# Kernel tuning notes

Measured on AMD Instinct MI355X. Metric: run time of the kernel, lower is better.

Reference implementation:

```python
import jax, jax.numpy as jnp
import numpy as np

B, IC, OC, K, H, W = 16, 16, 64, 3, 256, 256


def setup_inputs() -> dict:
    key = jax.random.key(0)
    k1, k2, k3 = jax.random.split(key, 3)
    x = jax.random.normal(k1, (B, IC, H, W), dtype=jnp.float32)
    # nn.Conv2d default init: uniform(-1/sqrt(fan_in), 1/sqrt(fan_in))
    bound = 1.0 / np.sqrt(IC * K * K)
    weight = jax.random.uniform(k2, (OC, IC, K, K), jnp.float32, -bound, bound)
    bias = jax.random.uniform(k3, (OC,), jnp.float32, -bound, bound)
    return {"x": x, "weight": weight, "bias": bias}


def reference(x, weight, bias):
    """Fused 'conv-window multiply -> min over (oc, kh, kw, ic) -> +bias -> tanh(tanh(.))'.

    Matches the CUDA kernel: for each output pixel it takes
        min over (oc, kh, kw, ic) of  x_pad[b, ic, h+kh, w+kw] * w[oc, ic, kh, kw] + bias[oc]
    (bias[oc] is constant within an oc, so folding it into the joint min is exact),
    then applies tanh twice. Output is [B, 1, H, W]; out-of-bounds taps use x=0
    (stride=1, padding=0 per the conv state, but the kernel still writes HxW).
    """
    b_, ic_, h_, w_ = x.shape
    oc_, _, k_, _ = weight.shape
    # zero-pad on the high side only: ih = ph + kh can reach H + K - 2
    xp = jnp.pad(x, ((0, 0), (0, 0), (0, k_ - 1), (0, k_ - 1)))

    # ---- pass 1: find the argmin index over the joint (oc, kh, kw, ic) axis ----
    xs = jax.lax.stop_gradient(xp)
    ws = jax.lax.stop_gradient(weight)
    bs = jax.lax.stop_gradient(bias)
    big = jnp.asarray(np.finfo(np.float32).max, jnp.float32)  # FLT_MAX as in kernel

    def body(carry, inp):
        best, bestj = carry                      # [B,H,W] f32, [B,H,W] i32
        wk, bk, oc = inp                         # [IC,K,K], scalar, i32
        for kh in range(k_):
            for kw in range(k_):
                win = xs[:, :, kh:kh + h_, kw:kw + w_]          # [B,IC,H,W]
                v = win * wk[None, :, kh, kw, None, None] + bk   # [B,IC,H,W]
                vm = jnp.min(v, axis=1)                          # [B,H,W]
                ici = jnp.argmin(v, axis=1).astype(jnp.int32)    # [B,H,W]
                jj = ((oc * k_ + kh) * k_ + kw) * ic_ + ici
                better = vm < best
                best = jnp.where(better, vm, best)
                bestj = jnp.where(better, jj, bestj)
        return (best, bestj), None

    init = (jnp.full((b_, h_, w_), big, jnp.float32),
            jnp.zeros((b_, h_, w_), jnp.int32))
    (_, bestj), _ = jax.lax.scan(body, init, (ws, bs, jnp.arange(oc_, dtype=jnp.int32)))

    # ---- pass 2: differentiable gather of the winning tap ----
    ic = bestj % ic_
    t = bestj // ic_
    kw = t % k_
    t = t // k_
    kh = t % k_
    oc = t // k_
    bi = jnp.arange(b_)[:, None, None]
    hi = jnp.arange(h_)[None, :, None]
    wi = jnp.arange(w_)[None, None, :]
    xv = xp[bi, ic, hi + kh, wi + kw]            # [B,H,W]
    wv = weight[oc, ic, kh, kw]                  # [B,H,W]
    out = jnp.tanh(jnp.tanh(xv * wv + bias[oc]))
    return out[:, None, :, :]                    # [B,1,H,W]
```

## Files before the change

kernel.cpp:

```cpp
#include <hip/hip_runtime.h>
#include <cmath>

constexpr int Bn = 16, ICn = 16, OCn = 64, Kn = 3, Hn = 256, Wn = 256;
constexpr int NE   = ICn * Kn * Kn;
constexpr int CAPF = 16;
constexpr int CNT_OFF   = 0;
constexpr int FLAG_OFF  = 256;
constexpr int LINES_OFF = 4096;

constexpr double XLIM = 16.0;

typedef float v2f __attribute__((ext_vector_type(2)));

__global__ void build_hulls(const float* __restrict__ weight,
                            const float* __restrict__ bias,
                            unsigned int* __restrict__ counts,
                            int* __restrict__ flag,
                            float2* __restrict__ lines)
{
    int wave = (int)(threadIdx.x >> 6);
    int lane = (int)(threadIdx.x & 63);
    int e = blockIdx.x * 4 + wave;
    if (e >= NE) return;
    int ic = e / (Kn * Kn);
    int t  = e % (Kn * Kn);

    double mm = (double)weight[((size_t)lane * ICn + ic) * (Kn * Kn) + t];
    double cc = (double)bias[lane];

    double v_cur = mm * (-XLIM) + cc;
    double m_cur = mm, c_cur = cc;
    #pragma unroll
    for (int off = 32; off >= 1; off >>= 1) {
        double v2 = __shfl_xor(v_cur, off, 64);
        double m2 = __shfl_xor(m_cur, off, 64);
        double c2 = __shfl_xor(c_cur, off, 64);
        if (v2 < v_cur || (v2 == v_cur && m2 < m_cur)) {
            v_cur = v2; m_cur = m2; c_cur = c2;
        }
    }

    float2* L = lines + (size_t)e * CAPF;
    int n = 0;
    while (true) {
        if (lane == 0 && n < CAPF) L[n] = make_float2((float)m_cur, (float)c_cur);
        ++n;
        double xi = 1e308, mi = 0.0, ci = 0.0;
        if (mm < m_cur) {
            xi = (cc - c_cur) / (m_cur - mm);
            mi = mm; ci = cc;
        }
        #pragma unroll
        for (int off = 32; off >= 1; off >>= 1) {
            double x2 = __shfl_xor(xi, off, 64);
            double m2 = __shfl_xor(mi, off, 64);
            double c2 = __shfl_xor(ci, off, 64);
            if (x2 < xi || (x2 == xi && (m2 < mi || (m2 == mi && c2 < ci)))) {
                xi = x2; mi = m2; ci = c2;
            }
        }
        if (xi >= XLIM) break;
        m_cur = mi; c_cur = ci;
    }
    if (lane == 0) {
        if (n > CAPF) { atomicOr(flag, 1); n = CAPF; }
        int np = (n + 3) & ~3;
        float2 last = L[n - 1];
        for (int p = n; p < np; ++p) L[p] = last;
        unsigned int g = (unsigned int)(np >> 2);
        atomicOr(&counts[ic * 2 + (t >> 3)], g << ((t & 7) * 4));
    }
}

__device__ __forceinline__ v2f vmin3(v2f a, v2f b, v2f c) {
    v2f r;
    r.x = fminf(a.x, fminf(b.x, c.x));
    r.y = fminf(a.y, fminf(b.y, c.y));
    return r;
}

__global__ __launch_bounds__(256) void fused_min_tanh4(
    const float* __restrict__ x,
    const unsigned int* __restrict__ counts,
    const int* __restrict__ flag,
    const float4* __restrict__ linesg,
    const float* __restrict__ weight,
    const float* __restrict__ bias,
    float* __restrict__ out)
{
    __shared__ float4 S[NE * (CAPF / 2)];
    __shared__ unsigned int Scw[32];

    const int tid = (int)threadIdx.x;
    for (int k = tid; k < NE * (CAPF / 2); k += 256) S[k] = linesg[k];
    if (tid < 32) Scw[tid] = counts[tid];
    __syncthreads();

    const int row  = (int)blockIdx.x * 4 + (tid >> 6);
    const int b0   = row >> 8;
    const int h    = row & 255;
    const int lane = tid & 63;
    const int w0   = lane << 2;
    const bool tail = (lane == 63);

    v2f A0, A1, A2, A3;
    A0.x = 3.4e38f; A0.y = 3.4e38f; A1 = A0; A2 = A0; A3 = A0;

    const float* xb = x + (size_t)b0 * (ICn * Hn * Wn);

    if (*flag == 0) {
        #pragma unroll 1
        for (int ic = 0; ic < ICn; ++ic) {
            const float* xc = xb + ic * (Hn * Wn);
            float r[3][6];
            #pragma unroll
            for (int kh = 0; kh < 3; ++kh) {
                const int hh = h + kh;
                if (hh < Hn) {
                    const float* rp = xc + hh * Wn;
                    const float4 Av = *reinterpret_cast<const float4*>(rp + w0);
                    const float2 Bv = *reinterpret_cast<const float2*>(
                                          tail ? (rp + w0) : (rp + w0 + 4));
                    r[kh][0] = Av.x; r[kh][1] = Av.y;
                    r[kh][2] = Av.z; r[kh][3] = Av.w;
                    r[kh][4] = tail ? 0.0f : Bv.x;
                    r[kh][5] = tail ? 0.0f : Bv.y;
                } else {
                    #pragma unroll
                    for (int j = 0; j < 6; ++j) r[kh][j] = 0.0f;
                }
            }
            const unsigned int cl = __builtin_amdgcn_readfirstlane(Scw[ic * 2]);
            const unsigned int ch = __builtin_amdgcn_readfirstlane(Scw[ic * 2 + 1]);
            #pragma unroll
            for (int kh = 0; kh < 3; ++kh) {
                #pragma unroll
                for (int kw = 0; kw < 3; ++kw) {
                    const int t9 = kh * 3 + kw;
                    const int e  = ic * 9 + t9;
                    const int g  = (int)(((t9 < 8) ? (cl >> (4 * t9))
                                                   : ch) & 15u);
                    const float4* Ls = &S[e * (CAPF / 2)];
                    v2f xx0, xx1;
                    xx0.x = r[kh][kw + 0]; xx0.y = r[kh][kw + 1];
                    xx1.x = r[kh][kw + 2]; xx1.y = r[kh][kw + 3];
                    for (int i = 0; i < g; ++i) {
                        const float4 u = Ls[2 * i + 0];
                        const float4 v = Ls[2 * i + 1];
                        A0 = vmin3(A0, xx0 * u.x + u.y, xx0 * u.z + u.w);
                        A1 = vmin3(A1, xx1 * u.x + u.y, xx1 * u.z + u.w);
                        A2 = vmin3(A2, xx0 * v.x + v.y, xx0 * v.z + v.w);
                        A3 = vmin3(A3, xx1 * v.x + v.y, xx1 * v.z + v.w);
                    }
                }
            }
        }
    } else {
        float best[4] = {3.4e38f, 3.4e38f, 3.4e38f, 3.4e38f};
        #pragma unroll 1
        for (int ic = 0; ic < ICn; ++ic) {
            const float* xc = xb + ic * (Hn * Wn);
            float r[3][6];
            #pragma unroll
            for (int kh = 0; kh < 3; ++kh) {
                const int hh = h + kh;
                if (hh < Hn) {
                    const float* rp = xc + hh * Wn;
                    const float4 Av = *reinterpret_cast<const float4*>(rp + w0);
                    const float2 Bv = *reinterpret_cast<const float2*>(
                                          tail ? (rp + w0) : (rp + w0 + 4));
                    r[kh][0] = Av.x; r[kh][1] = Av.y;
                    r[kh][2] = Av.z; r[kh][3] = Av.w;
                    r[kh][4] = tail ? 0.0f : Bv.x;
                    r[kh][5] = tail ? 0.0f : Bv.y;
                } else {
                    #pragma unroll
                    for (int j = 0; j < 6; ++j) r[kh][j] = 0.0f;
                }
            }
            for (int oc = 0; oc < OCn; ++oc) {
                const float bv = bias[oc];
                #pragma unroll
                for (int kh = 0; kh < 3; ++kh) {
                    #pragma unroll
                    for (int kw = 0; kw < 3; ++kw) {
                        const float wv =
                            weight[((size_t)(oc * ICn + ic) * Kn + kh) * Kn + kw];
                        #pragma unroll
                        for (int p = 0; p < 4; ++p)
                            best[p] = fminf(best[p],
                                            fmaf(r[kh][kw + p], wv, bv));
                    }
                }
            }
        }
        A0.x = best[0]; A0.y = best[1]; A1.x = best[2]; A1.y = best[3];
        A2 = A0; A3 = A1;
    }

    const float p0 = fminf(A0.x, A2.x);
    const float p1 = fminf(A0.y, A2.y);
    const float p2 = fminf(A1.x, A3.x);
    const float p3 = fminf(A1.y, A3.y);
    float4 o;
    o.x = tanhf(tanhf(p0));
    o.y = tanhf(tanhf(p1));
    o.z = tanhf(tanhf(p2));
    o.w = tanhf(tanhf(p3));
    *reinterpret_cast<float4*>(out + (((size_t)b0 * Hn + h) * Wn + w0)) = o;
}

__global__ __launch_bounds__(256) void brute_force(
    const float* __restrict__ x,
    const float* __restrict__ weight,
    const float* __restrict__ bias,
    float* __restrict__ out)
{
    int idx = blockIdx.x * 256 + (int)threadIdx.x;
    int w0 = idx & (Wn - 1);
    int h0 = (idx >> 8) & (Hn - 1);
    int b0 = idx >> 16;

    float best = 3.4e38f;
    const float* xb = x + ((size_t)b0 * ICn) * (Hn * Wn);
    for (int ic = 0; ic < ICn; ++ic) {
        const float* xc = xb + (size_t)ic * (Hn * Wn);
        #pragma unroll
        for (int kh = 0; kh < Kn; ++kh) {
            int hh = h0 + kh;
            #pragma unroll
            for (int kw = 0; kw < Kn; ++kw) {
                int ww = w0 + kw;
                float xvv = (hh < Hn && ww < Wn) ? xc[hh * Wn + ww] : 0.0f;
                for (int oc = 0; oc < OCn; ++oc) {
                    float wv = weight[((size_t)(oc * ICn + ic) * Kn + kh) * Kn + kw];
                    best = fminf(best, fmaf(xvv, wv, bias[oc]));
                }
            }
        }
    }
    out[idx] = tanhf(tanhf(best));
}

extern "C" void kernel_launch(void* const* d_in, const int* in_sizes, int n_in,
                              void* d_out, int out_size, void* d_ws, size_t ws_size,
                              hipStream_t stream)
{
    const float* x      = (const float*)d_in[0];
    const float* weight = (const float*)d_in[1];
    const float* bias   = (const float*)d_in[2];
    float* out = (float*)d_out;

    const size_t need = (size_t)LINES_OFF + (size_t)NE * CAPF * sizeof(float2);
    const int npix = Bn * Hn * Wn;

    if (ws_size >= need) {
        unsigned int* counts = (unsigned int*)((char*)d_ws + CNT_OFF);
        int*          flag   = (int*)((char*)d_ws + FLAG_OFF);
        float2*       lines  = (float2*)((char*)d_ws + LINES_OFF);
        hipMemsetAsync(d_ws, 0, 512, stream);
        build_hulls<<<dim3(NE / 4), dim3(256), 0, stream>>>(
            weight, bias, counts, flag, lines);
        fused_min_tanh4<<<dim3(Bn * Hn / 4), dim3(256), 0, stream>>>(
            x, counts, flag, (const float4*)lines, weight, bias, out);
    } else {
        brute_force<<<dim3(npix / 256), dim3(256), 0, stream>>>(
            x, weight, bias, out);
    }
}
```

Measured before the change: 88.57 us.

## Split input channels across blocks and merge partial minima with atomicMin

The main kernel now launches two blocks per row group, each covering half of the input channels. Their partial minima are combined in the output buffer with integer atomicMin on an order-preserving float-to-uint mapping, after the buffer is pre-filled with 0xFF. A separate kernel then unmaps the values and applies the double tanh. The hull lines are no longer staged in shared memory; they are read from global memory in a pre-packed float4 layout, with a software-pipelined load of the next line pair. This removes the per-block LDS fill and barrier and doubles block count, at the cost of an extra memset pass, atomic traffic and an extra elementwise kernel over the output.

```diff
diff --git a/kernel.cpp b/kernel.cpp
--- a/kernel.cpp
+++ b/kernel.cpp
@@ -7,16 +7,27 @@
 constexpr int CNT_OFF   = 0;
 constexpr int FLAG_OFF  = 256;
 constexpr int LINES_OFF = 4096;
+constexpr int TMP_OFF   = 32768;
 
 constexpr double XLIM = 16.0;
 
 typedef float v2f __attribute__((ext_vector_type(2)));
+
+__device__ __forceinline__ unsigned int fmap(float f) {
+    unsigned int b = __float_as_uint(f);
+    return (b & 0x80000000u) ? ~b : (b | 0x80000000u);
+}
+__device__ __forceinline__ float funmap(unsigned int u) {
+    unsigned int b = (u & 0x80000000u) ? (u ^ 0x80000000u) : ~u;
+    return __uint_as_float(b);
+}
 
 __global__ void build_hulls(const float* __restrict__ weight,
                             const float* __restrict__ bias,
                             unsigned int* __restrict__ counts,
                             int* __restrict__ flag,
-                            float2* __restrict__ lines)
+                            float4* __restrict__ lines4,
+                            float2* __restrict__ tmp)
 {
     int wave = (int)(threadIdx.x >> 6);
     int lane = (int)(threadIdx.x & 63);
@@ -40,7 +51,7 @@
         }
     }
 
-    float2* L = lines + (size_t)e * CAPF;
+    float2* L = tmp + (size_t)e * CAPF;
     int n = 0;
     while (true) {
         if (lane == 0 && n < CAPF) L[n] = make_float2((float)m_cur, (float)c_cur);
@@ -67,6 +78,11 @@
         int np = (n + 3) & ~3;
         float2 last = L[n - 1];
         for (int p = n; p < np; ++p) L[p] = last;
+        for (int j = 0; j < np / 2; ++j) {
+            float2 l0 = L[2 * j], l1 = L[2 * j + 1];
+            lines4[(size_t)e * (CAPF / 2) + j] =
+                make_float4(l0.x, l0.y, l1.x, l1.y);
+        }
         unsigned int g = (unsigned int)(np >> 2);
         atomicOr(&counts[ic * 2 + (t >> 3)], g << ((t & 7) * 4));
     }
@@ -79,29 +95,28 @@
     return r;
 }
 
-__global__ __launch_bounds__(256) void fused_min_tanh4(
+__global__ __launch_bounds__(256) void fused_min_atomic(
     const float* __restrict__ x,
     const unsigned int* __restrict__ counts,
     const int* __restrict__ flag,
-    const float4* __restrict__ linesg,
+    const float4* __restrict__ lines4,
     const float* __restrict__ weight,
     const float* __restrict__ bias,
-    float* __restrict__ out)
-{
-    __shared__ float4 S[NE * (CAPF / 2)];
-    __shared__ unsigned int Scw[32];
-
-    const int tid = (int)threadIdx.x;
-    for (int k = tid; k < NE * (CAPF / 2); k += 256) S[k] = linesg[k];
-    if (tid < 32) Scw[tid] = counts[tid];
-    __syncthreads();
-
-    const int row  = (int)blockIdx.x * 4 + (tid >> 6);
-    const int b0   = row >> 8;
-    const int h    = row & 255;
-    const int lane = tid & 63;
-    const int w0   = lane << 2;
-    const bool tail = (lane == 63);
+    unsigned int* __restrict__ outu)
+{
+    const int tid    = (int)threadIdx.x;
+    const int bid    = (int)blockIdx.x;
+    const int icHalf = bid & 1;
+    const int rg     = bid >> 1;
+    const int row    = rg * 4 + (tid >> 6);
+    const int b0     = row >> 8;
+    const int h      = row & 255;
+    const int lane   = tid & 63;
+    const int w0     = lane << 2;
+    const bool tail  = (lane == 63);
+    const int ic0    = icHalf * 8;
+
+    const unsigned int* cw = counts + (size_t)ic0 * 2;
 
     v2f A0, A1, A2, A3;
     A0.x = 3.4e38f; A0.y = 3.4e38f; A1 = A0; A2 = A0; A3 = A0;
@@ -110,7 +125,8 @@
 
     if (*flag == 0) {
         #pragma unroll 1
-        for (int ic = 0; ic < ICn; ++ic) {
+        for (int ici = 0; ici < 8; ++ici) {
+            const int ic = ic0 + ici;
             const float* xc = xb + ic * (Hn * Wn);
             float r[3][6];
             #pragma unroll
@@ -130,35 +146,41 @@
                     for (int j = 0; j < 6; ++j) r[kh][j] = 0.0f;
                 }
             }
-            const unsigned int cl = __builtin_amdgcn_readfirstlane(Scw[ic * 2]);
-            const unsigned int ch = __builtin_amdgcn_readfirstlane(Scw[ic * 2 + 1]);
+            const unsigned int cl = cw[ici * 2];
+            const unsigned int ch = cw[ici * 2 + 1];
             #pragma unroll
             for (int kh = 0; kh < 3; ++kh) {
                 #pragma unroll
                 for (int kw = 0; kw < 3; ++kw) {
                     const int t9 = kh * 3 + kw;
                     const int e  = ic * 9 + t9;
-                    const int g  = (int)(((t9 < 8) ? (cl >> (4 * t9))
-                                                   : ch) & 15u);
-                    const float4* Ls = &S[e * (CAPF / 2)];
-                    v2f xx0, xx1;
-                    xx0.x = r[kh][kw + 0]; xx0.y = r[kh][kw + 1];
-                    xx1.x = r[kh][kw + 2]; xx1.y = r[kh][kw + 3];
-                    for (int i = 0; i < g; ++i) {
-                        const float4 u = Ls[2 * i + 0];
-                        const float4 v = Ls[2 * i + 1];
-                        A0 = vmin3(A0, xx0 * u.x + u.y, xx0 * u.z + u.w);
-                        A1 = vmin3(A1, xx1 * u.x + u.y, xx1 * u.z + u.w);
-                        A2 = vmin3(A2, xx0 * v.x + v.y, xx0 * v.z + v.w);
-                        A3 = vmin3(A3, xx1 * v.x + v.y, xx1 * v.z + v.w);
+                    const int g  = (int)(((t9 < 8) ? (cl >> (4 * t9)) : ch) & 15u);
+                    const float4* L = lines4 + (size_t)e * (CAPF / 2);
+                    v2f x01, x23;
+                    x01.x = r[kh][kw + 0]; x01.y = r[kh][kw + 1];
+                    x23.x = r[kh][kw + 2]; x23.y = r[kh][kw + 3];
+                    float4 u = L[0];
+                    float4 v = L[1];
+                    for (int i = 1; i < g; ++i) {
+                        const float4 un = L[2 * i + 0];
+                        const float4 vn = L[2 * i + 1];
+                        A0 = vmin3(A0, x01 * u.x + u.y, x01 * u.z + u.w);
+                        A2 = vmin3(A2, x23 * u.x + u.y, x23 * u.z + u.w);
+                        A1 = vmin3(A1, x01 * v.x + v.y, x01 * v.z + v.w);
+                        A3 = vmin3(A3, x23 * v.x + v.y, x23 * v.z + v.w);
+                        u = un; v = vn;
                     }
+                    A0 = vmin3(A0, x01 * u.x + u.y, x01 * u.z + u.w);
+                    A2 = vmin3(A2, x23 * u.x + u.y, x23 * u.z + u.w);
+                    A1 = vmin3(A1, x01 * v.x + v.y, x01 * v.z + v.w);
+                    A3 = vmin3(A3, x23 * v.x + v.y, x23 * v.z + v.w);
                 }
             }
         }
     } else {
-        float best[4] = {3.4e38f, 3.4e38f, 3.4e38f, 3.4e38f};
         #pragma unroll 1
-        for (int ic = 0; ic < ICn; ++ic) {
+        for (int ici = 0; ici < 8; ++ici) {
+            const int ic = ic0 + ici;
             const float* xc = xb + ic * (Hn * Wn);
             float r[3][6];
             #pragma unroll
@@ -186,28 +208,34 @@
                     for (int kw = 0; kw < 3; ++kw) {
                         const float wv =
                             weight[((size_t)(oc * ICn + ic) * Kn + kh) * Kn + kw];
-                        #pragma unroll
-                        for (int p = 0; p < 4; ++p)
-                            best[p] = fminf(best[p],
-                                            fmaf(r[kh][kw + p], wv, bv));
+                        A0.x = fminf(A0.x, fmaf(r[kh][kw + 0], wv, bv));
+                        A0.y = fminf(A0.y, fmaf(r[kh][kw + 1], wv, bv));
+                        A2.x = fminf(A2.x, fmaf(r[kh][kw + 2], wv, bv));
+                        A2.y = fminf(A2.y, fmaf(r[kh][kw + 3], wv, bv));
                     }
                 }
             }
         }
-        A0.x = best[0]; A0.y = best[1]; A1.x = best[2]; A1.y = best[3];
-        A2 = A0; A3 = A1;
-    }
-
-    const float p0 = fminf(A0.x, A2.x);
-    const float p1 = fminf(A0.y, A2.y);
-    const float p2 = fminf(A1.x, A3.x);
-    const float p3 = fminf(A1.y, A3.y);
-    float4 o;
-    o.x = tanhf(tanhf(p0));
-    o.y = tanhf(tanhf(p1));
-    o.z = tanhf(tanhf(p2));
-    o.w = tanhf(tanhf(p3));
-    *reinterpret_cast<float4*>(out + (((size_t)b0 * Hn + h) * Wn + w0)) = o;
+    }
+
+    const float p0 = fminf(A0.x, A1.x);
+    const float p1 = fminf(A0.y, A1.y);
+    const float p2 = fminf(A2.x, A3.x);
+    const float p3 = fminf(A2.y, A3.y);
+
+    unsigned int* op = outu + (((size_t)b0 * Hn + h) * Wn + w0);
+    atomicMin(op + 0, fmap(p0));
+    atomicMin(op + 1, fmap(p1));
+    atomicMin(op + 2, fmap(p2));
+    atomicMin(op + 3, fmap(p3));
+}
+
+__global__ __launch_bounds__(256) void map_tanh(unsigned int* __restrict__ u,
+                                                float* __restrict__ f)
+{
+    const int idx = (int)blockIdx.x * 256 + (int)threadIdx.x;
+    const float v = funmap(u[idx]);
+    f[idx] = tanhf(tanhf(v));
 }
 
 __global__ __launch_bounds__(256) void brute_force(
@@ -251,18 +279,25 @@
     const float* bias   = (const float*)d_in[2];
     float* out = (float*)d_out;
 
-    const size_t need = (size_t)LINES_OFF + (size_t)NE * CAPF * sizeof(float2);
+    const size_t need = (size_t)TMP_OFF + (size_t)NE * CAPF * sizeof(float2);
     const int npix = Bn * Hn * Wn;
 
     if (ws_size >= need) {
         unsigned int* counts = (unsigned int*)((char*)d_ws + CNT_OFF);
         int*          flag   = (int*)((char*)d_ws + FLAG_OFF);
-        float2*       lines  = (float2*)((char*)d_ws + LINES_OFF);
+        float4*       lines4 = (float4*)((char*)d_ws + LINES_OFF);
+        float2*       tmp    = (float2*)((char*)d_ws + TMP_OFF);
+
         hipMemsetAsync(d_ws, 0, 512, stream);
         build_hulls<<<dim3(NE / 4), dim3(256), 0, stream>>>(
-            weight, bias, counts, flag, lines);
-        fused_min_tanh4<<<dim3(Bn * Hn / 4), dim3(256), 0, stream>>>(
-            x, counts, flag, (const float4*)lines, weight, bias, out);
+            weight, bias, counts, flag, lines4, tmp);
+
+        hipMemsetAsync(d_out, 0xFF, (size_t)npix * 4, stream);
+        fused_min_atomic<<<dim3(npix / 1024 * 2), dim3(256), 0, stream>>>(
+            x, counts, flag, lines4, weight, bias, (unsigned int*)d_out);
+
+        map_tanh<<<dim3(npix / 256), dim3(256), 0, stream>>>(
+            (unsigned int*)d_out, out);
     } else {
         brute_force<<<dim3(npix / 256), dim3(256), 0, stream>>>(
             x, weight, bias, out);
```

After: 85.26 us. 1.04x faster.
